# Optimization experiments

Measured on AMD Instinct MI355X. Metric: run time of the kernel, lower is better.

Reference implementation:

```python
import jax, jax.numpy as jnp
import numpy as np

C = 1.0          # curvature
SQC = 1.0        # sqrt(c)
MIN_NORM = 1e-15
PROJ_EPS = 4e-3  # float32 boundary eps (HGCN convention)

def _norm(x):
    return jnp.clip(jnp.linalg.norm(x, axis=-1, keepdims=True), MIN_NORM)

def logmap0(x):
    n = _norm(x)
    return jnp.arctanh(jnp.minimum(SQC * n, 1.0 - 1e-7)) * x / (SQC * n)

def expmap0(u):
    n = _norm(u)
    return jnp.tanh(SQC * n) * u / (SQC * n)

def proj(x):
    n = _norm(x)
    maxn = (1.0 - PROJ_EPS) / SQC
    return jnp.where(n > maxn, x / n * maxn, x)

def mobius_add(x, y):
    x2 = jnp.sum(x * x, -1, keepdims=True)
    y2 = jnp.sum(y * y, -1, keepdims=True)
    xy = jnp.sum(x * y, -1, keepdims=True)
    num = (1.0 + 2.0 * C * xy + C * y2) * x + (1.0 - C * x2) * y
    den = 1.0 + 2.0 * C * xy + C * C * x2 * y2
    return num / jnp.clip(den, MIN_NORM)

N, E, DIN, H, DH = 50000, 800000, 256, 4, 64  # heads*DH == out_features == 256

def setup_inputs() -> dict:
    key = jax.random.key(0)
    k1, k2, k3, k4, k5, k6, k7 = jax.random.split(key, 7)
    x = proj(0.01 * jax.random.normal(k1, (N, DIN), jnp.float32))  # points on the ball
    src = jax.random.randint(k2, (E,), 0, N)
    off = jax.random.randint(k3, (E,), 1, N)
    dst = (src + off) % N  # no self loops (remove_self_loops); added in reference
    edge_index = jnp.stack([src, dst]).astype(jnp.int64)
    glorot = float(np.sqrt(2.0 / (DIN + H * DH)))
    W = glorot * jax.random.normal(k4, (H * DH, DIN), jnp.float32)
    b_lin = 0.01 * jax.random.normal(k5, (H * DH,), jnp.float32)
    ga = float(np.sqrt(6.0 / (1 + 2 * DH)))
    att = jax.random.uniform(k6, (H, 2 * DH), jnp.float32, -ga, ga)
    b_conv = jnp.zeros((H * DH,), jnp.float32)
    return {"x": x, "edge_index": edge_index, "W": W, "b_lin": b_lin,
            "att": att, "b_conv": b_conv}

def reference(x, edge_index, W, b_lin, att, b_conv):
    n = x.shape[0]
    # HypLinear: mobius_matvec + hyperbolic bias (dropout=0, eval)
    xh = proj(expmap0(logmap0(x) @ W.T))
    hb = proj(expmap0(b_lin[None, :]))
    xh = proj(mobius_add(xh, hb))
    # add self loops (edge_index already has none)
    loop = jnp.arange(n)
    src = jnp.concatenate([edge_index[0], loop])
    dst = jnp.concatenate([edge_index[1], loop])
    # faithful to original: logmap0 then view(heads, -1, out_ch)
    logx = logmap0(xh).reshape(H, n, DH)  # [H,N,DH]
    # per-edge attention logits via per-node partial scores (same math as cat@att)
    s_i = jnp.einsum('hnd,hd->nh', logx, att[:, :DH])
    s_j = jnp.einsum('hnd,hd->nh', logx, att[:, DH:])
    alpha = jax.nn.leaky_relu(s_i[dst] + s_j[src], 0.2)  # [Etot,H]
    # segment softmax over incoming edges of each target node
    m = jax.ops.segment_max(alpha, dst, num_segments=n)
    a = jnp.exp(alpha - m[dst])
    ssum = jax.ops.segment_sum(a, dst, num_segments=n)
    a = a / jnp.clip(ssum[dst], MIN_NORM)
    # gather source messages, weight, scatter-add
    xj = jnp.take(logx, src, axis=1).transpose(1, 0, 2)  # [Etot,H,DH]
    out = jax.ops.segment_sum(xj * a[:, :, None], dst, num_segments=n)  # [N,H,DH]
    # faithful to original update(): [H,N,DH].view(-1, H*DH) + bias
    out = out.transpose(1, 0, 2).reshape(n, H * DH) + b_conv
    out = jax.nn.relu(out)  # act between proj_tan0 (identity for Poincare)
    return proj(expmap0(out))
```

## Files before the change

### kernel.cpp

```cpp
#include <hip/hip_runtime.h>

#define MIN_NORM 1e-15f
#define MAXN (1.0f - 4e-3f)

typedef __attribute__((ext_vector_type(8))) short short8;
typedef __attribute__((ext_vector_type(4))) float f32x4;

__device__ __forceinline__ float bf2f(unsigned short u) {
  union { unsigned int i; float f; } c; c.i = ((unsigned int)u) << 16; return c.f;
}
__device__ __forceinline__ unsigned short f2bf(float f) {
  union { float f; unsigned int i; } c; c.f = f;
  unsigned int r = c.i + 0x7FFFu + ((c.i >> 16) & 1u);
  return (unsigned short)(r >> 16);
}
__device__ __forceinline__ float wave_sum(float v) {
#pragma unroll
  for (int off = 32; off > 0; off >>= 1) v += __shfl_xor(v, off, 64);
  return v;
}
__device__ __forceinline__ float gsum16(float v) {
#pragma unroll
  for (int off = 8; off > 0; off >>= 1) v += __shfl_xor(v, off, 64);
  return v;
}

__global__ __launch_bounds__(256) void k_prep(const float* __restrict__ x,
                                              const float* __restrict__ W,
                                              const float* __restrict__ b_lin,
                                              float* __restrict__ rs,
                                              unsigned short* __restrict__ xb,
                                              unsigned short* __restrict__ Wb,
                                              float* __restrict__ hb,
                                              float* __restrict__ hb2,
                                              int* __restrict__ cnt,
                                              unsigned short* __restrict__ slots, int N) {
  int row = blockIdx.x * 4 + (threadIdx.x >> 6);
  int lane = threadIdx.x & 63;
  float4 u = *(const float4*)(x + (size_t)row * 256 + lane * 4);
  ushort4 st;
  st.x = f2bf(u.x); st.y = f2bf(u.y); st.z = f2bf(u.z); st.w = f2bf(u.w);
  *(ushort4*)(xb + (size_t)row * 256 + lane * 4) = st;
  float s = wave_sum(u.x * u.x + u.y * u.y + u.z * u.z + u.w * u.w);
  if (lane == 0) {
    float n = fmaxf(sqrtf(s), MIN_NORM);
    rs[row] = atanhf(fminf(n, 1.0f - 1e-7f)) / n;
  }
  int g = blockIdx.x * 256 + threadIdx.x;
  if (g < N) { cnt[g] = 1; slots[(size_t)g * 64] = (unsigned short)g; }
  if (blockIdx.x < 64) {
    int idx = (blockIdx.x * 256 + threadIdx.x) * 4;
    float4 wv = *(const float4*)(W + idx);
    ushort4 ws;
    ws.x = f2bf(wv.x); ws.y = f2bf(wv.y); ws.z = f2bf(wv.z); ws.w = f2bf(wv.w);
    *(ushort4*)(Wb + idx) = ws;
  }
  if (blockIdx.x == 64 && threadIdx.x < 64) {
    float4 b4 = ((const float4*)b_lin)[lane];
    float bx = b4.x, by = b4.y, bz = b4.z, bw = b4.w;
    float sb = wave_sum(bx * bx + by * by + bz * bz + bw * bw);
    float n1 = fmaxf(sqrtf(sb), MIN_NORM);
    float t = tanhf(n1) / n1;
    bx *= t; by *= t; bz *= t; bw *= t;
    float s2 = wave_sum(bx * bx + by * by + bz * bz + bw * bw);
    float n2 = fmaxf(sqrtf(s2), MIN_NORM);
    if (n2 > MAXN) { float f = MAXN / n2; bx *= f; by *= f; bz *= f; bw *= f; }
    float4 o; o.x = bx; o.y = by; o.z = bz; o.w = bw;
    ((float4*)hb)[lane] = o;
    float s3 = wave_sum(bx * bx + by * by + bz * bz + bw * bw);
    if (lane == 0) *hb2 = s3;
  }
}

__global__ __launch_bounds__(256) void k_gemmhyp(const unsigned short* __restrict__ xb,
                                                 const unsigned short* __restrict__ Wb,
                                                 const float* __restrict__ rs,
                                                 const float* __restrict__ hb,
                                                 const float* __restrict__ hb2p,
                                                 const float* __restrict__ att,
                                                 unsigned short* __restrict__ L,
                                                 float* __restrict__ s_i,
                                                 float* __restrict__ s_j,
                                                 int M, int NQ) {
  int tid = threadIdx.x;
  int wv = tid >> 6, lane = tid & 63, qd = lane >> 4, lc = lane & 15;
  int i0 = blockIdx.x * 64;
  int arow = i0 + wv * 16 + lc;
  if (arow >= M) arow = M - 1;
  short8 af[8];
#pragma unroll
  for (int kk = 0; kk < 8; ++kk)
    af[kk] = *(const short8*)(xb + (size_t)arow * 256 + kk * 32 + qd * 8);
  f32x4 acc[16];
#pragma unroll
  for (int jt = 0; jt < 16; ++jt) acc[jt] = (f32x4){0.f, 0.f, 0.f, 0.f};
#pragma unroll
  for (int kk = 0; kk < 8; ++kk) {
#pragma unroll
    for (int half = 0; half < 2; ++half) {
      short8 bf[8];
#pragma unroll
      for (int j = 0; j < 8; ++j)
        bf[j] = *(const short8*)(Wb + (size_t)((half * 8 + j) * 16 + lc) * 256 + kk * 32 + qd * 8);
#pragma unroll
      for (int j = 0; j < 8; ++j)
        acc[half * 8 + j] =
            __builtin_amdgcn_mfma_f32_16x16x32_bf16(af[kk], bf[j], acc[half * 8 + j], 0, 0, 0);
    }
  }
  float y2 = *hb2p;
  float hbreg[16];
#pragma unroll
  for (int jt = 0; jt < 16; ++jt) hbreg[jt] = hb[jt * 16 + lc];

#pragma unroll
  for (int r = 0; r < 4; ++r) {
    int row_r = i0 + wv * 16 + qd * 4 + r;
    bool valid = row_r < M;
    int rr = valid ? row_r : M - 1;
    float rsv = rs[rr];
    float v[16];
    float ss = 0.0f;
#pragma unroll
    for (int jt = 0; jt < 16; ++jt) { v[jt] = rsv * acc[jt][r]; ss += v[jt] * v[jt]; }
    ss = gsum16(ss);
    float n1 = fmaxf(sqrtf(ss), MIN_NORM);
    float e1 = tanhf(n1) / n1;
    float n2 = e1 * n1;
    float f2 = (n2 > MAXN) ? MAXN / n2 : 1.0f;
    float e12 = e1 * f2;
    float nx = n2 * f2;
    float x2 = nx * nx;
#pragma unroll
    for (int jt = 0; jt < 16; ++jt) v[jt] *= e12;
    float xy = 0.0f;
#pragma unroll
    for (int jt = 0; jt < 16; ++jt) xy += v[jt] * hbreg[jt];
    xy = gsum16(xy);
    float c1 = 1.0f + 2.0f * xy + y2;
    float c2 = 1.0f - x2;
    float den = fmaxf(1.0f + 2.0f * xy + x2 * y2, MIN_NORM);
    float inv = 1.0f / den;
    float s3 = inv * inv * (c1 * c1 * x2 + 2.0f * c1 * c2 * xy + c2 * c2 * y2);
    float n3 = fmaxf(sqrtf(s3), MIN_NORM);
    float f3 = (n3 > MAXN) ? MAXN / n3 : 1.0f;
    float n4 = fmaxf(n3 * f3, MIN_NORM);
    float sc = atanhf(n4) / n4;
    float g = inv * f3 * sc;
    float Lv[16];
#pragma unroll
    for (int jt = 0; jt < 16; ++jt) Lv[jt] = (c1 * v[jt] + c2 * hbreg[jt]) * g;
    int h_r = row_r / NQ;
    int q_r = row_r - h_r * NQ;
    if (valid) {
#pragma unroll
      for (int jt = 0; jt < 16; ++jt) {
        int n = q_r * 4 + (jt >> 2);
        int d = (jt & 3) * 16 + lc;
        L[(size_t)n * 256 + h_r * 64 + d] = f2bf(Lv[jt]);
      }
    }
    float pig[4], pjg[4];
#pragma unroll
    for (int g4 = 0; g4 < 4; ++g4) {
      float pi = 0.0f, pj = 0.0f;
#pragma unroll
      for (int t = 0; t < 4; ++t) {
        float a_i = att[h_r * 128 + t * 16 + lc];
        float a_j = att[h_r * 128 + 64 + t * 16 + lc];
        pi += Lv[g4 * 4 + t] * a_i;
        pj += Lv[g4 * 4 + t] * a_j;
      }
      pig[g4] = gsum16(pi);
      pjg[g4] = gsum16(pj);
    }
    if (valid && lc == 0) {
#pragma unroll
      for (int g4 = 0; g4 < 4; ++g4) {
        int n = q_r * 4 + g4;
        s_i[n * 4 + h_r] = pig[g4];
        s_j[n * 4 + h_r] = pjg[g4];
      }
    }
  }
}

__global__ void k_fill(const int* __restrict__ ei, int* __restrict__ cnt,
                       unsigned short* __restrict__ slots, int E) {
  int e = blockIdx.x * blockDim.x + threadIdx.x;
  if (e < E) {
    int s = ei[e];
    int d = ei[E + e];
    int pos = atomicAdd(&cnt[d], 1);
    if (pos < 64) slots[(size_t)d * 64 + pos] = (unsigned short)s;
  }
}

__global__ __launch_bounds__(256) void HGATLayer_49246095016355_kernel(
    const unsigned short* __restrict__ L,
    const float* __restrict__ s_i,
    const float* __restrict__ s_j,
    const int* __restrict__ cnt,
    const unsigned short* __restrict__ slots,
    const float* __restrict__ b_conv,
    float* __restrict__ out, int N, int NQ) {
  int q = blockIdx.x;
  int w = threadIdx.x >> 6, lane = threadIdx.x & 63;
  int n = q * 4 + w;
  int deg = min(cnt[n], 64);
  float4 si4 = *(const float4*)(s_i + n * 4);
  int src_l = n;
  float4 a4 = {-1e30f, -1e30f, -1e30f, -1e30f};
  if (lane < deg) {
    src_l = slots[(size_t)n * 64 + lane];
    float4 sj4 = *(const float4*)(s_j + src_l * 4);
    float t0 = si4.x + sj4.x, t1 = si4.y + sj4.y, t2 = si4.z + sj4.z, t3 = si4.w + sj4.w;
    a4.x = (t0 > 0.f) ? t0 : 0.2f * t0;
    a4.y = (t1 > 0.f) ? t1 : 0.2f * t1;
    a4.z = (t2 > 0.f) ? t2 : 0.2f * t2;
    a4.w = (t3 > 0.f) ? t3 : 0.2f * t3;
  }
  float4 mx = a4;
#pragma unroll
  for (int off = 32; off > 0; off >>= 1) {
    mx.x = fmaxf(mx.x, __shfl_xor(mx.x, off, 64));
    mx.y = fmaxf(mx.y, __shfl_xor(mx.y, off, 64));
    mx.z = fmaxf(mx.z, __shfl_xor(mx.z, off, 64));
    mx.w = fmaxf(mx.w, __shfl_xor(mx.w, off, 64));
  }
  float4 p4 = {0.f, 0.f, 0.f, 0.f};
  if (lane < deg) {
    p4.x = __expf(a4.x - mx.x); p4.y = __expf(a4.y - mx.y);
    p4.z = __expf(a4.z - mx.z); p4.w = __expf(a4.w - mx.w);
  }
  float4 sm = p4;
#pragma unroll
  for (int off = 32; off > 0; off >>= 1) {
    sm.x += __shfl_xor(sm.x, off, 64);
    sm.y += __shfl_xor(sm.y, off, 64);
    sm.z += __shfl_xor(sm.z, off, 64);
    sm.w += __shfl_xor(sm.w, off, 64);
  }
  __shared__ int   s_src[4][64];
  __shared__ float s_w[4][64][4];
  s_src[w][lane] = src_l;
  *(float4*)&s_w[w][lane][0] = p4;

  int c = lane & 31, ep = lane >> 5, hc = c >> 3;
  float smh = (hc == 0) ? sm.x : (hc == 1) ? sm.y : (hc == 2) ? sm.z : sm.w;

  float accv[8];
#pragma unroll
  for (int j = 0; j < 8; ++j) accv[j] = 0.f;
  int np2 = (deg + 1) >> 1;
  int nb = (np2 + 7) >> 3;
  for (int b = 0; b < nb; ++b) {
    int kbase = b * 16 + ep;
    int ks[8];
#pragma unroll
    for (int p = 0; p < 8; ++p) ks[p] = s_src[w][kbase + 2 * p];
    short8 r[8];
#pragma unroll
    for (int p = 0; p < 8; ++p)
      r[p] = *(const short8*)(L + (size_t)ks[p] * 256 + c * 8);
    float wk[8];
#pragma unroll
    for (int p = 0; p < 8; ++p) wk[p] = s_w[w][kbase + 2 * p][hc];
#pragma unroll
    for (int p = 0; p < 8; ++p) {
#pragma unroll
      for (int j = 0; j < 8; ++j)
        accv[j] = fmaf(wk[p], bf2f((unsigned short)r[p][j]), accv[j]);
    }
  }
#pragma unroll
  for (int j = 0; j < 8; ++j) accv[j] += __shfl_xor(accv[j], 32, 64);

  float isum = 1.0f / fmaxf(smh, MIN_NORM);
  const float* bcp = b_conv + w * 64 + (c & 7) * 8;
  float vv[8];
  float ps = 0.f;
#pragma unroll
  for (int j = 0; j < 8; ++j) {
    float t = fmaxf(accv[j] * isum + bcp[j], 0.0f);
    vv[j] = t;
    ps += t * t;
  }
#pragma unroll
  for (int off = 1; off < 8; off <<= 1) ps += __shfl_xor(ps, off, 64);
  __shared__ float red[4][4];
  if (lane < 32 && (c & 7) == 0) red[w][hc] = ps;
  __syncthreads();
  float tot = red[0][hc] + red[1][hc] + red[2][hc] + red[3][hc];
  float nraw = sqrtf(tot);
  float ncl = fmaxf(nraw, MIN_NORM);
  float t = tanhf(ncl) / ncl;
  float ny = fmaxf(t * nraw, MIN_NORM);
  float f = (ny > MAXN) ? (MAXN / ny) : 1.0f;
  float tf = t * f;
  if (lane < 32) {
    float4 y0; y0.x = tf * vv[0]; y0.y = tf * vv[1]; y0.z = tf * vv[2]; y0.w = tf * vv[3];
    float4 y1; y1.x = tf * vv[4]; y1.y = tf * vv[5]; y1.z = tf * vv[6]; y1.w = tf * vv[7];
    float* op = out + (size_t)(hc * NQ + q) * 256 + w * 64 + (c & 7) * 8;
    *(float4*)op = y0;
    *(float4*)(op + 4) = y1;
  }
}

extern "C" void kernel_launch(void* const* d_in, const int* in_sizes, int n_in,
                              void* d_out, int out_size, void* d_ws, size_t ws_size,
                              hipStream_t stream) {
  const float* x   = (const float*)d_in[0];
  const int*   ei  = (const int*)d_in[1];
  const float* W   = (const float*)d_in[2];
  const float* bl  = (const float*)d_in[3];
  const float* att = (const float*)d_in[4];
  const float* bc  = (const float*)d_in[5];
  float* out = (float*)d_out;

  const int N = in_sizes[0] / 256;
  const int E = in_sizes[1] / 2;
  const int NQ = N / 4;

  unsigned short* xb = (unsigned short*)d_out;

  char* w = (char*)d_ws;
  unsigned short* L  = (unsigned short*)w; w += (size_t)N * 256 * 2;
  unsigned short* Wb = (unsigned short*)w; w += 65536 * 2;
  float* s_i = (float*)w; w += (size_t)N * 4 * 4;
  float* s_j = (float*)w; w += (size_t)N * 4 * 4;
  float* rs  = (float*)w; w += (size_t)N * 4;
  float* hb  = (float*)w; w += 256 * 4;
  float* hb2 = (float*)w; w += 16;
  int* cnt   = (int*)w;   w += (size_t)N * 4;
  unsigned short* slots = (unsigned short*)w;

  k_prep<<<N / 4, 256, 0, stream>>>(x, W, bl, rs, xb, Wb, hb, hb2, cnt, slots, N);
  k_gemmhyp<<<(N + 63) / 64, 256, 0, stream>>>(xb, Wb, rs, hb, hb2, att, L, s_i, s_j, N, NQ);
  k_fill<<<(E + 255) / 256, 256, 0, stream>>>(ei, cnt, slots, E);
  HGATLayer_49246095016355_kernel<<<NQ, 256, 0, stream>>>(L, s_i, s_j, cnt, slots, bc, out, N, NQ);
}
```

Measured before the change: 306.4 us.

## Merge edge fill into GEMM launch and pre-swizzle W into MFMA fragment layout

The edge-fill pass (atomic degree counting and slot writes) now runs as extra blocks of the GEMM kernel instead of a separate launch, so the two independent workloads can share the GPU and one launch disappears. W is also converted to bf16 in a fragment-ordered layout, letting each lane load its B operand with one contiguous, fully coalesced 16-byte read instead of strided row reads. The fill blocks are scheduled after the GEMM blocks in the same grid and compete with them for CU resources and registers, since the fused kernel keeps the GEMM's register allocation.

```diff
diff --git a/kernel.cpp b/kernel.cpp
--- a/kernel.cpp
+++ b/kernel.cpp
@@ -48,12 +48,17 @@
   }
   int g = blockIdx.x * 256 + threadIdx.x;
   if (g < N) { cnt[g] = 1; slots[(size_t)g * 64] = (unsigned short)g; }
-  if (blockIdx.x < 64) {
-    int idx = (blockIdx.x * 256 + threadIdx.x) * 4;
-    float4 wv = *(const float4*)(W + idx);
-    ushort4 ws;
-    ws.x = f2bf(wv.x); ws.y = f2bf(wv.y); ws.z = f2bf(wv.z); ws.w = f2bf(wv.w);
-    *(ushort4*)(Wb + idx) = ws;
+  if (blockIdx.x < 32) {
+    int g2 = blockIdx.x * 256 + threadIdx.x;
+    int ln = g2 & 63, fj = g2 >> 6;
+    int kk = fj >> 4, hf = (fj >> 3) & 1, j = fj & 7;
+    int lc2 = ln & 15, qd2 = ln >> 4;
+    const float* src = W + (size_t)(((hf * 8 + j) * 16 + lc2) * 256 + kk * 32 + qd2 * 8);
+    float4 a = *(const float4*)src;
+    float4 b = *(const float4*)(src + 4);
+    unsigned short* dst = Wb + (size_t)g2 * 8;
+    dst[0] = f2bf(a.x); dst[1] = f2bf(a.y); dst[2] = f2bf(a.z); dst[3] = f2bf(a.w);
+    dst[4] = f2bf(b.x); dst[5] = f2bf(b.y); dst[6] = f2bf(b.z); dst[7] = f2bf(b.w);
   }
   if (blockIdx.x == 64 && threadIdx.x < 64) {
     float4 b4 = ((const float4*)b_lin)[lane];
@@ -72,16 +77,29 @@
   }
 }
 
-__global__ __launch_bounds__(256) void k_gemmhyp(const unsigned short* __restrict__ xb,
-                                                 const unsigned short* __restrict__ Wb,
-                                                 const float* __restrict__ rs,
-                                                 const float* __restrict__ hb,
-                                                 const float* __restrict__ hb2p,
-                                                 const float* __restrict__ att,
-                                                 unsigned short* __restrict__ L,
-                                                 float* __restrict__ s_i,
-                                                 float* __restrict__ s_j,
-                                                 int M, int NQ) {
+__global__ __launch_bounds__(256) void k_gemmfill(const unsigned short* __restrict__ xb,
+                                                  const unsigned short* __restrict__ Wb,
+                                                  const float* __restrict__ rs,
+                                                  const float* __restrict__ hb,
+                                                  const float* __restrict__ hb2p,
+                                                  const float* __restrict__ att,
+                                                  unsigned short* __restrict__ L,
+                                                  float* __restrict__ s_i,
+                                                  float* __restrict__ s_j,
+                                                  const int* __restrict__ ei,
+                                                  int* __restrict__ cnt,
+                                                  unsigned short* __restrict__ slots,
+                                                  int E, int GB, int M, int NQ) {
+  if (blockIdx.x >= GB) {
+    int e = (blockIdx.x - GB) * 256 + threadIdx.x;
+    if (e < E) {
+      int s = ei[e];
+      int d = ei[E + e];
+      int pos = atomicAdd(&cnt[d], 1);
+      if (pos < 64) slots[(size_t)d * 64 + pos] = (unsigned short)s;
+    }
+    return;
+  }
   int tid = threadIdx.x;
   int wv = tid >> 6, lane = tid & 63, qd = lane >> 4, lc = lane & 15;
   int i0 = blockIdx.x * 64;
@@ -101,7 +119,7 @@
       short8 bf[8];
 #pragma unroll
       for (int j = 0; j < 8; ++j)
-        bf[j] = *(const short8*)(Wb + (size_t)((half * 8 + j) * 16 + lc) * 256 + kk * 32 + qd * 8);
+        bf[j] = *(const short8*)(Wb + (size_t)(((kk * 2 + half) * 8 + j) * 64 + lane) * 8);
 #pragma unroll
       for (int j = 0; j < 8; ++j)
         acc[half * 8 + j] =
@@ -182,17 +200,6 @@
         s_j[n * 4 + h_r] = pjg[g4];
       }
     }
-  }
-}
-
-__global__ void k_fill(const int* __restrict__ ei, int* __restrict__ cnt,
-                       unsigned short* __restrict__ slots, int E) {
-  int e = blockIdx.x * blockDim.x + threadIdx.x;
-  if (e < E) {
-    int s = ei[e];
-    int d = ei[E + e];
-    int pos = atomicAdd(&cnt[d], 1);
-    if (pos < 64) slots[(size_t)d * 64 + pos] = (unsigned short)s;
   }
 }
 
@@ -335,8 +342,11 @@
   int* cnt   = (int*)w;   w += (size_t)N * 4;
   unsigned short* slots = (unsigned short*)w;
 
+  const int GB = (N + 63) / 64;
+  const int FB = (E + 255) / 256;
+
   k_prep<<<N / 4, 256, 0, stream>>>(x, W, bl, rs, xb, Wb, hb, hb2, cnt, slots, N);
-  k_gemmhyp<<<(N + 63) / 64, 256, 0, stream>>>(xb, Wb, rs, hb, hb2, att, L, s_i, s_j, N, NQ);
-  k_fill<<<(E + 255) / 256, 256, 0, stream>>>(ei, cnt, slots, E);
+  k_gemmfill<<<GB + FB, 256, 0, stream>>>(xb, Wb, rs, hb, hb2, att, L, s_i, s_j,
+                                          ei, cnt, slots, E, GB, N, NQ);
   HGATLayer_49246095016355_kernel<<<NQ, 256, 0, stream>>>(L, s_i, s_j, cnt, slots, bc, out, N, NQ);
 }
```

Result: faster. 254.4 us (-17.0%).
